# Kernel optimization log

Hardware: AMD Instinct MI355X
Metric: run time of the kernel (lower is better)

The kernel has to match this reference:

```python
import jax, jax.numpy as jnp
import numpy as np

N_NODES = 50000
N_EDGES = 800000
D_IN = 256
D_OUT = 128
EPS = 1e-9


def setup_inputs() -> dict:
    key = jax.random.key(0)
    ks = jax.random.split(key, 6)
    feat = jax.random.normal(ks[0], (N_NODES, D_IN), dtype=jnp.float32)
    edge_row = jax.random.randint(ks[1], (N_EDGES,), 0, N_NODES)
    edge_col = jax.random.randint(ks[2], (N_EDGES,), 0, N_NODES)
    # normalized adjacency values (positive, ~1/degree scale)
    edge_val = jax.random.uniform(ks[3], (N_EDGES,), dtype=jnp.float32) / 16.0
    # xavier_uniform for Linear(dim_in, dim_out) weights, stored as [D_IN, D_OUT]
    limit = float(np.sqrt(6.0 / (D_IN + D_OUT)))
    W0 = jax.random.uniform(ks[4], (D_IN, D_OUT), minval=-limit, maxval=limit, dtype=jnp.float32)
    W1 = jax.random.uniform(ks[5], (D_IN, D_OUT), minval=-limit, maxval=limit, dtype=jnp.float32)
    zeros = jnp.zeros((D_OUT,), dtype=jnp.float32)
    ones = jnp.ones((D_OUT,), dtype=jnp.float32)
    return {
        "feat": feat,
        "W0": W0, "b0": zeros, "scale0": ones, "offset0": zeros,
        "W1": W1, "b1": zeros, "scale1": ones, "offset1": zeros,
        "edge_row": edge_row, "edge_col": edge_col, "edge_val": edge_val,
    }


def _spmm(edge_row, edge_col, edge_val, x):
    # out[r] += val * x[c] for each edge (r, c, val)  -- sparse adj @ x
    msgs = edge_val[:, None] * x[edge_col]  # [E, D]
    return jax.ops.segment_sum(msgs, edge_row, num_segments=N_NODES)


def _feat_trans(x, W, b, scale, offset):
    h = jax.nn.relu(x @ W + b)  # [N, D_OUT]
    mean = jnp.mean(h, axis=1, keepdims=True)
    var = jnp.var(h, axis=1, keepdims=True) + EPS  # unbiased=False (population var)
    return (h - mean) * scale * jax.lax.rsqrt(var) + offset


def reference(feat, W0, b0, scale0, offset0, W1, b1, scale1, offset1,
              edge_row, edge_col, edge_val):
    # non-first-layer path: feat_hop = [X, A @ X] (order=1), dropout p=0 is identity
    hop1 = _spmm(edge_row, edge_col, edge_val, feat)
    f0 = _feat_trans(feat, W0, b0, scale0, offset0)
    f1 = _feat_trans(hop1, W1, b1, scale1, offset1)
    return jnp.concatenate([f0, f1], axis=1)  # aggr == 'concat'
```

## Files before the change

kernel.cpp:

```cpp
#include <hip/hip_runtime.h>

#define N_NODES 50000
#define N_EDGES 800000
#define D_IN    256
#define D_OUT   128
#define EPS     1e-9f
#define BPAD    136

#define SCATTER_BLOCKS 196
#define GEMM_MBLKS     391

#define RPB    64
#define NBUCK  782
#define BCAP   1344
#define GSTR   16

typedef __attribute__((ext_vector_type(8))) short bf16x8;
typedef __attribute__((ext_vector_type(4))) float floatx4;

__device__ __forceinline__ ushort f2bf(float x) {
    unsigned u = __float_as_uint(x);
    u += 0x7fffu + ((u >> 16) & 1u);
    return (ushort)(u >> 16);
}

__device__ __forceinline__ bf16x8 packbf(float4 a, float4 b) {
    union { ushort us[8]; bf16x8 v; } r;
    r.us[0] = f2bf(a.x); r.us[1] = f2bf(a.y);
    r.us[2] = f2bf(a.z); r.us[3] = f2bf(a.w);
    r.us[4] = f2bf(b.x); r.us[5] = f2bf(b.y);
    r.us[6] = f2bf(b.z); r.us[7] = f2bf(b.w);
    return r.v;
}

#define WB_BLOCKS  32
__global__ __launch_bounds__(256) void prep_small(
    const float* __restrict__ W0, const float* __restrict__ W1,
    ushort* __restrict__ Wb, int* __restrict__ gcnt)
{
    int bid = blockIdx.x;
    int t   = threadIdx.x;
    if (bid == 0) {
        for (int i = t; i < NBUCK * GSTR; i += 256) gcnt[i] = 0;
    } else {
        int g  = (bid - 1) * 256 + t;
        int n  = g >> 5;
        int kq = g & 31;
        const float* W = (n < 128) ? W0 : W1;
        int nn = n & 127;
        union { ushort us[8]; uint4 v; } tmp;
#pragma unroll
        for (int j = 0; j < 8; ++j)
            tmp.us[j] = f2bf(W[(size_t)(kq * 8 + j) * D_OUT + nn]);
        *(uint4*)&Wb[(size_t)n * D_IN + kq * 8] = tmp.v;
    }
}

__global__ __launch_bounds__(512, 4) void gemm_scatter(
    const float* __restrict__ feat, const ushort* __restrict__ Wb,
    const float* __restrict__ bias, const float* __restrict__ scale,
    const float* __restrict__ offset,
    float* __restrict__ out, ushort* __restrict__ Y1,
    const int* __restrict__ er, const int* __restrict__ ec,
    const float* __restrict__ ev, int* __restrict__ gcnt,
    uint2* __restrict__ bedge)
{
    __shared__ __align__(16) ushort Bs[128 * BPAD];

    const int t = threadIdx.x;

    if (blockIdx.x < SCATTER_BLOCKS) {
        int* hist = (int*)Bs;
        int* base = hist + NBUCK;
        for (int i = t; i < NBUCK; i += 512) hist[i] = 0;
        __syncthreads();

        int ebase = blockIdx.x * 4096;
        int   bkt[8], rnk[8];
        uint2 pk[8];
#pragma unroll
        for (int u = 0; u < 8; ++u) {
            int e = ebase + u * 512 + t;
            bool ok = (e < N_EDGES);
            int   r = ok ? er[e] : 0;
            int   c = ok ? ec[e] : 0;
            float v = ok ? ev[e] : 0.f;
            bkt[u] = ok ? (r >> 6) : -1;
            pk[u]  = make_uint2(((unsigned)(r & 63) << 16) | (unsigned)c,
                                __float_as_uint(v));
            if (ok) rnk[u] = atomicAdd(&hist[r >> 6], 1);
        }
        __syncthreads();
        for (int i = t; i < NBUCK; i += 512) {
            int h = hist[i];
            base[i] = h ? atomicAdd(&gcnt[i * GSTR], h) : 0;
        }
        __syncthreads();
#pragma unroll
        for (int u = 0; u < 8; ++u) {
            if (bkt[u] >= 0) {
                int pos = base[bkt[u]] + rnk[u];
                if (pos < BCAP)
                    bedge[(size_t)bkt[u] * BCAP + pos] = pk[u];
            }
        }
        return;
    }

    const int gbid = blockIdx.x - SCATTER_BLOCKS;
    const int half = gbid / GEMM_MBLKS;
    const int mblk = gbid % GEMM_MBLKS;
    const int wave = t >> 6, lane = t & 63;
    const int quad = lane >> 4, l16 = lane & 15;
    const int m0   = mblk * 128;
    const int n0   = half * 128;

    const int grow = m0 + wave * 16 + l16;
    const int arow = grow < N_NODES ? grow : 0;
    const float* aptr = &feat[(size_t)arow * D_IN + quad * 8];

    floatx4 acc[8];
#pragma unroll
    for (int nt = 0; nt < 8; ++nt)
        acc[nt] = (floatx4){0.f, 0.f, 0.f, 0.f};

    for (int kt = 0; kt < D_IN; kt += 128) {
#pragma unroll
        for (int i = 0; i < 8; ++i) {
            int g = t + i * 512;
            int row = g >> 4, kq = g & 15;
            *(uint4*)&Bs[row * BPAD + kq * 8] =
                *(const uint4*)&Wb[(size_t)(n0 + row) * D_IN + kt + kq * 8];
        }
        __syncthreads();

        const float* p = aptr + kt;
        float4 q0 = *(const float4*)(p +  0), q1 = *(const float4*)(p +  4);
        float4 q2 = *(const float4*)(p + 32), q3 = *(const float4*)(p + 36);
        float4 q4 = *(const float4*)(p + 64), q5 = *(const float4*)(p + 68);
        float4 q6 = *(const float4*)(p + 96), q7 = *(const float4*)(p + 100);
        bf16x8 a0 = packbf(q0, q1), a1 = packbf(q2, q3);
        bf16x8 a2 = packbf(q4, q5), a3 = packbf(q6, q7);

#pragma unroll
        for (int s = 0; s < 4; ++s) {
            bf16x8 a = (s == 0) ? a0 : (s == 1) ? a1 : (s == 2) ? a2 : a3;
            const int kk = s * 32;
            bf16x8 b[8];
#pragma unroll
            for (int nt = 0; nt < 8; ++nt)
                b[nt] = *(bf16x8*)&Bs[(nt * 16 + l16) * BPAD + kk + quad * 8];
#pragma unroll
            for (int nt = 0; nt < 8; ++nt)
                acc[nt] = __builtin_amdgcn_mfma_f32_16x16x32_bf16(
                    a, b[nt], acc[nt], 0, 0, 0);
        }
        __syncthreads();
    }

    if (half == 0) {
        float bb[8], sc[8], of[8];
#pragma unroll
        for (int nt = 0; nt < 8; ++nt) {
            bb[nt] = bias[nt * 16 + l16];
            sc[nt] = scale[nt * 16 + l16];
            of[nt] = offset[nt * 16 + l16];
        }
#pragma unroll
        for (int i = 0; i < 4; ++i) {
            float h[8], s = 0.f, q = 0.f;
#pragma unroll
            for (int nt = 0; nt < 8; ++nt) {
                h[nt] = fmaxf(acc[nt][i] + bb[nt], 0.f);
                s += h[nt];
                q += h[nt] * h[nt];
            }
#pragma unroll
            for (int m = 1; m < 16; m <<= 1) {
                s += __shfl_xor(s, m);
                q += __shfl_xor(q, m);
            }
            float mean = s * (1.f / 128.f);
            float inv  = rsqrtf(q * (1.f / 128.f) - mean * mean + EPS);
            int row = m0 + wave * 16 + quad * 4 + i;
            if (row < N_NODES) {
#pragma unroll
                for (int nt = 0; nt < 8; ++nt)
                    out[(size_t)row * 256 + nt * 16 + l16] =
                        (h[nt] - mean) * sc[nt] * inv + of[nt];
            }
        }
    } else {
#pragma unroll
        for (int i = 0; i < 4; ++i) {
            int row = m0 + wave * 16 + quad * 4 + i;
            if (row < N_NODES) {
#pragma unroll
                for (int nt = 0; nt < 8; ++nt)
                    Y1[(size_t)row * D_OUT + nt * 16 + l16] =
                        f2bf(acc[nt][i]);
            }
        }
    }
}

__global__ __launch_bounds__(512) void spmm_csr_ln(
    const int* __restrict__ gcnt, const uint2* __restrict__ bedge,
    const ushort* __restrict__ Y,
    const float* __restrict__ bias, const float* __restrict__ scale,
    const float* __restrict__ offset, float* __restrict__ out)
{
    __shared__ ushort lcol[BCAP];
    __shared__ float  lval[BCAP];
    __shared__ int    cnt[RPB];
    __shared__ int    offx[RPB];

    const int t      = threadIdx.x;
    const int bucket = blockIdx.x;
    const int r0     = bucket * RPB;
    const int nrows  = min(RPB, N_NODES - r0);
    int ne = gcnt[bucket * GSTR];
    ne = ne < BCAP ? ne : BCAP;

    if (t < RPB) cnt[t] = 0;
    __syncthreads();

    const size_t base = (size_t)bucket * BCAP;
    int   erA = -1, erB = -1, erC = -1;
    int   ecA = 0,  ecB = 0,  ecC = 0;
    float evA = 0.f, evB = 0.f, evC = 0.f;
    int   rkA = 0,  rkB = 0,  rkC = 0;
    if (t < ne) {
        uint2 p = bedge[base + t];
        erA = (int)(p.x >> 16); ecA = (int)(p.x & 0xffffu);
        evA = __uint_as_float(p.y);
        rkA = atomicAdd(&cnt[erA], 1);
    }
    if (t + 512 < ne) {
        uint2 p = bedge[base + t + 512];
        erB = (int)(p.x >> 16); ecB = (int)(p.x & 0xffffu);
        evB = __uint_as_float(p.y);
        rkB = atomicAdd(&cnt[erB], 1);
    }
    if (t + 1024 < ne) {
        uint2 p = bedge[base + t + 1024];
        erC = (int)(p.x >> 16); ecC = (int)(p.x & 0xffffu);
        evC = __uint_as_float(p.y);
        rkC = atomicAdd(&cnt[erC], 1);
    }
    __syncthreads();

    if (t < RPB) {
        int c = cnt[t], x = c;
#pragma unroll
        for (int s = 1; s < RPB; s <<= 1) {
            int w = __shfl_up(x, s);
            if (t >= s) x += w;
        }
        offx[t] = x - c;
    }
    __syncthreads();

    if (erA >= 0) { int k = offx[erA] + rkA; lcol[k] = (ushort)ecA; lval[k] = evA; }
    if (erB >= 0) { int k = offx[erB] + rkB; lcol[k] = (ushort)ecB; lval[k] = evB; }
    if (erC >= 0) { int k = offx[erC] + rkC; lcol[k] = (ushort)ecC; lval[k] = evC; }
    __syncthreads();

    const int wave = t >> 6, lane = t & 63;
    const int cidx = lane * 2;
    const float b0v = bias[cidx],   b1v = bias[cidx + 1];
    const float s0v = scale[cidx],  s1v = scale[cidx + 1];
    const float o0v = offset[cidx], o1v = offset[cidx + 1];

    for (int ri = wave; ri < nrows; ri += 8) {
        int beg = offx[ri], n = cnt[ri];
        float ax = 0.f, ay = 0.f;
        for (int j = 0; j < n; j += 16) {
            unsigned yv[16]; float vv[16];
#pragma unroll
            for (int u = 0; u < 16; ++u) {
                int jj  = j + u;
                bool ok = jj < n;
                int idx = beg + (ok ? jj : 0);
                int c   = lcol[idx];
                vv[u]   = ok ? lval[idx] : 0.f;
                yv[u]   = *(const unsigned*)&Y[(size_t)c * D_OUT + cidx];
            }
#pragma unroll
            for (int u = 0; u < 16; ++u) {
                ax = fmaf(vv[u], __uint_as_float(yv[u] << 16), ax);
                ay = fmaf(vv[u], __uint_as_float(yv[u] & 0xffff0000u), ay);
            }
        }
        float h0 = fmaxf(ax + b0v, 0.f);
        float h1 = fmaxf(ay + b1v, 0.f);
        float s = h0 + h1, q = h0 * h0 + h1 * h1;
#pragma unroll
        for (int m = 1; m < 64; m <<= 1) {
            s += __shfl_xor(s, m);
            q += __shfl_xor(q, m);
        }
        float mean = s * (1.f / 128.f);
        float inv  = rsqrtf(q * (1.f / 128.f) - mean * mean + EPS);
        int row = r0 + ri;
        float2 o;
        o.x = (h0 - mean) * s0v * inv + o0v;
        o.y = (h1 - mean) * s1v * inv + o1v;
        *(float2*)&out[(size_t)row * 256 + 128 + cidx] = o;
    }
}

extern "C" void kernel_launch(void* const* d_in, const int* in_sizes, int n_in,
                              void* d_out, int out_size, void* d_ws, size_t ws_size,
                              hipStream_t stream)
{
    const float* feat = (const float*)d_in[0];
    const float* W0   = (const float*)d_in[1];
    const float* b0   = (const float*)d_in[2];
    const float* s0   = (const float*)d_in[3];
    const float* o0   = (const float*)d_in[4];
    const float* W1   = (const float*)d_in[5];
    const float* b1   = (const float*)d_in[6];
    const float* s1   = (const float*)d_in[7];
    const float* o1   = (const float*)d_in[8];
    const int*   er   = (const int*)d_in[9];
    const int*   ec   = (const int*)d_in[10];
    const float* ev   = (const float*)d_in[11];
    float* out = (float*)d_out;

    char*   wsb   = (char*)d_ws;
    ushort* Wb    = (ushort*)(wsb);
    ushort* Y1    = (ushort*)(wsb + 131072);
    int*    gcnt  = (int*)   (wsb + 12931072);
    uint2*  bedge = (uint2*) (wsb + 12981248);

    prep_small<<<1 + WB_BLOCKS, 256, 0, stream>>>(W0, W1, Wb, gcnt);

    gemm_scatter<<<SCATTER_BLOCKS + 2 * GEMM_MBLKS, 512, 0, stream>>>(
        feat, Wb, b0, s0, o0, out, Y1, er, ec, ev, gcnt, bedge);

    spmm_csr_ln<<<NBUCK, 512, 0, stream>>>(
        gcnt, bedge, Y1, b1, s1, o1, out);
}
```

Baseline: 190.5 us.

## Locally sort scattered edges by bucket and pad per-row CSR segments

In the scatter blocks, edges are now counting-sorted by bucket in shared memory using a block-wide prefix scan, then written to global bedge in sorted order so consecutive threads write contiguous addresses. In the SpMM kernel, each row's edge segment is padded to a multiple of 8 with zeroed entries, and column offsets are stored pre-scaled as byte offsets. This removes per-iteration bounds checks and index arithmetic in the gather loop. The cost is more shared memory and extra syncs in the scatter phase, plus zeroing the LDS edge buffer.

```diff
diff --git a/kernel.cpp b/kernel.cpp
--- a/kernel.cpp
+++ b/kernel.cpp
@@ -14,6 +14,15 @@
 #define NBUCK  782
 #define BCAP   1344
 #define GSTR   16
+#define LCAP   1792
+
+#define SORT_OFF  0
+#define HIST_OFF  32768
+#define LOFF_OFF  35896
+#define BASE_OFF  39024
+#define CSUM_OFF  42152
+#define CBAS_OFF  42216
+#define SMEM_BYTES 42280
 
 typedef __attribute__((ext_vector_type(8))) short bf16x8;
 typedef __attribute__((ext_vector_type(4))) float floatx4;
@@ -65,17 +74,23 @@
     const float* __restrict__ ev, int* __restrict__ gcnt,
     uint2* __restrict__ bedge)
 {
-    __shared__ __align__(16) ushort Bs[128 * BPAD];
+    __shared__ __align__(16) char smem[SMEM_BYTES];
 
     const int t = threadIdx.x;
 
     if (blockIdx.x < SCATTER_BLOCKS) {
-        int* hist = (int*)Bs;
-        int* base = hist + NBUCK;
+        uint2* sorted = (uint2*)(smem + SORT_OFF);
+        int*   hist   = (int*)(smem + HIST_OFF);
+        int*   loff   = (int*)(smem + LOFF_OFF);
+        int*   base   = (int*)(smem + BASE_OFF);
+        int*   csum   = (int*)(smem + CSUM_OFF);
+        int*   cbas   = (int*)(smem + CBAS_OFF);
+
         for (int i = t; i < NBUCK; i += 512) hist[i] = 0;
         __syncthreads();
 
-        int ebase = blockIdx.x * 4096;
+        const int ebase  = blockIdx.x * 4096;
+        const int ecount = min(4096, N_EDGES - ebase);
         int   bkt[8], rnk[8];
         uint2 pk[8];
 #pragma unroll
@@ -85,23 +100,66 @@
             int   r = ok ? er[e] : 0;
             int   c = ok ? ec[e] : 0;
             float v = ok ? ev[e] : 0.f;
-            bkt[u] = ok ? (r >> 6) : -1;
-            pk[u]  = make_uint2(((unsigned)(r & 63) << 16) | (unsigned)c,
+            int   b = r >> 6;
+            bkt[u] = ok ? b : -1;
+            pk[u]  = make_uint2(((unsigned)b << 22) |
+                                ((unsigned)(r & 63) << 16) | (unsigned)c,
                                 __float_as_uint(v));
-            if (ok) rnk[u] = atomicAdd(&hist[r >> 6], 1);
-        }
-        __syncthreads();
+            if (ok) rnk[u] = atomicAdd(&hist[b], 1);
+        }
+        __syncthreads();
+
+        {
+            const int lane = t & 63, w = t >> 6;
+            int v0 = (t < NBUCK) ? hist[t] : 0;
+            int x0 = v0;
+#pragma unroll
+            for (int s = 1; s < 64; s <<= 1) {
+                int y = __shfl_up(x0, s);
+                if (lane >= s) x0 += y;
+            }
+            if (lane == 63) csum[w] = x0;
+            const int i1 = t + 512;
+            int v1 = (i1 < NBUCK) ? hist[i1] : 0;
+            int x1 = v1;
+#pragma unroll
+            for (int s = 1; s < 64; s <<= 1) {
+                int y = __shfl_up(x1, s);
+                if (lane >= s) x1 += y;
+            }
+            if (lane == 63) csum[8 + w] = x1;
+            __syncthreads();
+            if (t == 0) {
+                int run = 0;
+#pragma unroll
+                for (int c = 0; c < 16; ++c) { cbas[c] = run; run += csum[c]; }
+            }
+            __syncthreads();
+            if (t < NBUCK)  loff[t]  = x0 - v0 + cbas[w];
+            if (i1 < NBUCK) loff[i1] = x1 - v1 + cbas[8 + w];
+        }
+        __syncthreads();
+
+#pragma unroll
+        for (int u = 0; u < 8; ++u) {
+            if (bkt[u] >= 0)
+                sorted[loff[bkt[u]] + rnk[u]] = pk[u];
+        }
         for (int i = t; i < NBUCK; i += 512) {
             int h = hist[i];
             base[i] = h ? atomicAdd(&gcnt[i * GSTR], h) : 0;
         }
         __syncthreads();
+
 #pragma unroll
         for (int u = 0; u < 8; ++u) {
-            if (bkt[u] >= 0) {
-                int pos = base[bkt[u]] + rnk[u];
+            int k = t + u * 512;
+            if (k < ecount) {
+                uint2 e = sorted[k];
+                int b   = (int)(e.x >> 22);
+                int pos = base[b] + (k - loff[b]);
                 if (pos < BCAP)
-                    bedge[(size_t)bkt[u] * BCAP + pos] = pk[u];
+                    bedge[(size_t)b * BCAP + pos] = e;
             }
         }
         return;
@@ -114,6 +172,7 @@
     const int quad = lane >> 4, l16 = lane & 15;
     const int m0   = mblk * 128;
     const int n0   = half * 128;
+    ushort* Bs = (ushort*)smem;
 
     const int grow = m0 + wave * 16 + l16;
     const int arow = grow < N_NODES ? grow : 0;
@@ -210,10 +269,10 @@
     const float* __restrict__ bias, const float* __restrict__ scale,
     const float* __restrict__ offset, float* __restrict__ out)
 {
-    __shared__ ushort lcol[BCAP];
-    __shared__ float  lval[BCAP];
-    __shared__ int    cnt[RPB];
-    __shared__ int    offx[RPB];
+    __shared__ uint2 lds_e[LCAP];
+    __shared__ int   cnt[RPB];
+    __shared__ int   offx[RPB];
+    __shared__ int   cntp[RPB];
 
     const int t      = threadIdx.x;
     const int bucket = blockIdx.x;
@@ -223,73 +282,82 @@
     ne = ne < BCAP ? ne : BCAP;
 
     if (t < RPB) cnt[t] = 0;
+    {
+        uint4* ez = (uint4*)lds_e;
+        ez[t] = make_uint4(0u, 0u, 0u, 0u);
+        if (t + 512 < 896) ez[t + 512] = make_uint4(0u, 0u, 0u, 0u);
+    }
     __syncthreads();
 
     const size_t base = (size_t)bucket * BCAP;
     int   erA = -1, erB = -1, erC = -1;
-    int   ecA = 0,  ecB = 0,  ecC = 0;
-    float evA = 0.f, evB = 0.f, evC = 0.f;
+    unsigned exA = 0, exB = 0, exC = 0;
+    unsigned evA = 0, evB = 0, evC = 0;
     int   rkA = 0,  rkB = 0,  rkC = 0;
     if (t < ne) {
         uint2 p = bedge[base + t];
-        erA = (int)(p.x >> 16); ecA = (int)(p.x & 0xffffu);
-        evA = __uint_as_float(p.y);
+        erA = (int)((p.x >> 16) & 63u); exA = (p.x & 0xffffu) << 8;
+        evA = p.y;
         rkA = atomicAdd(&cnt[erA], 1);
     }
     if (t + 512 < ne) {
         uint2 p = bedge[base + t + 512];
-        erB = (int)(p.x >> 16); ecB = (int)(p.x & 0xffffu);
-        evB = __uint_as_float(p.y);
+        erB = (int)((p.x >> 16) & 63u); exB = (p.x & 0xffffu) << 8;
+        evB = p.y;
         rkB = atomicAdd(&cnt[erB], 1);
     }
     if (t + 1024 < ne) {
         uint2 p = bedge[base + t + 1024];
-        erC = (int)(p.x >> 16); ecC = (int)(p.x & 0xffffu);
-        evC = __uint_as_float(p.y);
+        erC = (int)((p.x >> 16) & 63u); exC = (p.x & 0xffffu) << 8;
+        evC = p.y;
         rkC = atomicAdd(&cnt[erC], 1);
     }
     __syncthreads();
 
     if (t < RPB) {
-        int c = cnt[t], x = c;
+        int c  = cnt[t];
+        int cp = (c + 7) & ~7;
+        int x  = cp;
 #pragma unroll
         for (int s = 1; s < RPB; s <<= 1) {
             int w = __shfl_up(x, s);
             if (t >= s) x += w;
         }
-        offx[t] = x - c;
+        offx[t] = x - cp;
+        cntp[t] = cp;
     }
     __syncthreads();
 
-    if (erA >= 0) { int k = offx[erA] + rkA; lcol[k] = (ushort)ecA; lval[k] = evA; }
-    if (erB >= 0) { int k = offx[erB] + rkB; lcol[k] = (ushort)ecB; lval[k] = evB; }
-    if (erC >= 0) { int k = offx[erC] + rkC; lcol[k] = (ushort)ecC; lval[k] = evC; }
+    if (erA >= 0) lds_e[offx[erA] + rkA] = make_uint2(exA, evA);
+    if (erB >= 0) lds_e[offx[erB] + rkB] = make_uint2(exB, evB);
+    if (erC >= 0) lds_e[offx[erC] + rkC] = make_uint2(exC, evC);
     __syncthreads();
 
-    const int wave = t >> 6, lane = t & 63;
-    const int cidx = lane * 2;
+    const int wave  = t >> 6, lane = t & 63;
+    const int lane4 = lane * 4;
+    const int cidx  = lane * 2;
+    const char* Yb  = (const char*)Y;
     const float b0v = bias[cidx],   b1v = bias[cidx + 1];
     const float s0v = scale[cidx],  s1v = scale[cidx + 1];
     const float o0v = offset[cidx], o1v = offset[cidx + 1];
 
     for (int ri = wave; ri < nrows; ri += 8) {
-        int beg = offx[ri], n = cnt[ri];
+        int beg = offx[ri], np = cntp[ri];
         float ax = 0.f, ay = 0.f;
-        for (int j = 0; j < n; j += 16) {
-            unsigned yv[16]; float vv[16];
-#pragma unroll
-            for (int u = 0; u < 16; ++u) {
-                int jj  = j + u;
-                bool ok = jj < n;
-                int idx = beg + (ok ? jj : 0);
-                int c   = lcol[idx];
-                vv[u]   = ok ? lval[idx] : 0.f;
-                yv[u]   = *(const unsigned*)&Y[(size_t)c * D_OUT + cidx];
-            }
-#pragma unroll
-            for (int u = 0; u < 16; ++u) {
-                ax = fmaf(vv[u], __uint_as_float(yv[u] << 16), ax);
-                ay = fmaf(vv[u], __uint_as_float(yv[u] & 0xffff0000u), ay);
+        for (int j = 0; j < np; j += 8) {
+            uint2 e[8];
+#pragma unroll
+            for (int u = 0; u < 8; ++u)
+                e[u] = lds_e[beg + j + u];
+            unsigned yv[8];
+#pragma unroll
+            for (int u = 0; u < 8; ++u)
+                yv[u] = *(const unsigned*)(Yb + e[u].x + lane4);
+#pragma unroll
+            for (int u = 0; u < 8; ++u) {
+                float v = __uint_as_float(e[u].y);
+                ax = fmaf(v, __uint_as_float(yv[u] << 16), ax);
+                ay = fmaf(v, __uint_as_float(yv[u] & 0xffff0000u), ay);
             }
         }
         float h0 = fmaxf(ax + b0v, 0.f);
```

Result: faster. 173.9 us (-8.7%).
